# Kernel tuning notes

Hardware: AMD Instinct MI355X
Metric: run time of the kernel (lower is better)

Reference implementation:

```python
import jax, jax.numpy as jnp
import numpy as np

B, S, DIM, NH = 2, 2048, 1536, 12
HD = DIM // NH            # 128
C = HD // 2               # 64 rotary pairs
CF = C - 2 * (C // 3)     # 22 (frame axis)
CH = C // 3               # 21 (height axis)
CW = C // 3               # 21 (width axis)
GF, GH, GW = 8, 16, 16    # grid sizes, GF*GH*GW == S
EPS = 1e-6


def _freq_table(n_pos, dim):
    inv = 1.0 / (10000.0 ** (np.arange(dim, dtype=np.float64) / dim))
    ang = np.outer(np.arange(n_pos, dtype=np.float64), inv)
    return (np.cos(ang).astype(np.float32), np.sin(ang).astype(np.float32))


def setup_inputs() -> dict:
    key = jax.random.key(0)
    ks = jax.random.split(key, 8)
    scale = 0.02
    cos_f, sin_f = _freq_table(GF, CF)
    cos_h, sin_h = _freq_table(GH, CH)
    cos_w, sin_w = _freq_table(GW, CW)
    return {
        'x': jax.random.normal(ks[0], (B, S, DIM), dtype=jnp.float32),
        'seq_lens': jnp.array([2048, 1600], dtype=jnp.int32),
        'f': GF, 'h': GH, 'w': GW,
        'wq': scale * jax.random.normal(ks[1], (DIM, DIM), dtype=jnp.float32),
        'bq': jnp.zeros((DIM,), jnp.float32),
        'wk': scale * jax.random.normal(ks[2], (DIM, DIM), dtype=jnp.float32),
        'bk': jnp.zeros((DIM,), jnp.float32),
        'wv': scale * jax.random.normal(ks[3], (DIM, DIM), dtype=jnp.float32),
        'bv': jnp.zeros((DIM,), jnp.float32),
        'wo': scale * jax.random.normal(ks[4], (DIM, DIM), dtype=jnp.float32),
        'bo': jnp.zeros((DIM,), jnp.float32),
        'nq_w': jnp.ones((DIM,), jnp.float32),
        'nk_w': jnp.ones((DIM,), jnp.float32),
        'cos_f': jnp.asarray(cos_f), 'sin_f': jnp.asarray(sin_f),
        'cos_h': jnp.asarray(cos_h), 'sin_h': jnp.asarray(sin_h),
        'cos_w': jnp.asarray(cos_w), 'sin_w': jnp.asarray(sin_w),
    }


def _rmsnorm(t, wt):
    return t * jax.lax.rsqrt(jnp.mean(t * t, axis=-1, keepdims=True) + EPS) * wt


def _grid_rope(t, cos, sin, b, s):
    # t: [b, s, NH, HD] ; cos/sin: [s, 1, C] (per-position assembled freqs)
    tp = t.reshape(b, s, NH, C, 2)
    xr, xi = tp[..., 0], tp[..., 1]
    rr = xr * cos - xi * sin          # complex multiply by e^{i*theta}
    ri = xr * sin + xi * cos
    return jnp.stack([rr, ri], axis=-1).reshape(b, s, NH, HD)


def reference(x, seq_lens, f, h, w, wq, bq, wk, bk, wv, bv, wo, bo,
              nq_w, nk_w, cos_f, sin_f, cos_h, sin_h, cos_w, sin_w):
    b, s, _ = x.shape
    # QKV projections with RMSNorm on q/k over full dim (as in the module)
    q = _rmsnorm(x @ wq.T + bq, nq_w).reshape(b, s, NH, HD)
    k = _rmsnorm(x @ wk.T + bk, nk_w).reshape(b, s, NH, HD)
    v = (x @ wv.T + bv).reshape(b, s, NH, HD)
    # grid-indexed RoPE: zero offsets / target==grid => arange sampling per axis
    idx = jnp.arange(s)
    fi = idx // (h * w)
    hi = (idx // w) % h
    wi = idx % w
    cos = jnp.concatenate([cos_f[fi], cos_h[hi], cos_w[wi]], axis=-1)[:, None, :]
    sin = jnp.concatenate([sin_f[fi], sin_h[hi], sin_w[wi]], axis=-1)[:, None, :]
    qr = _grid_rope(q, cos, sin, b, s)
    kr = _grid_rope(k, cos, sin, b, s)
    # attention with ragged key-length masking (flash_attention k_lens)
    scale = 1.0 / jnp.sqrt(jnp.float32(HD))
    scores = jnp.einsum('bqnd,bknd->bnqk', qr, kr) * scale
    kmask = idx[None, :] < seq_lens[:, None]            # [b, s]
    scores = jnp.where(kmask[:, None, None, :], scores, jnp.float32(-1e30))
    attn = jax.nn.softmax(scores, axis=-1)
    out = jnp.einsum('bnqk,bknd->bqnd', attn, v).reshape(b, s, DIM)
    return out @ wo.T + bo
```

## Files before the change

kernel.cpp:

```cpp
#include <hip/hip_runtime.h>
#include <hip/hip_bf16.h>
#include <math.h>

#define DIM_  1536
#define NH_   12
#define HD_   128
#define S_    2048
#define B_    2
#define M_    (B_*S_)
#define WEL_  (DIM_*DIM_)

typedef __attribute__((ext_vector_type(8))) _Float16 f16x8;
typedef __attribute__((ext_vector_type(4))) short short4v;
typedef __attribute__((ext_vector_type(8))) short short8v;
typedef __attribute__((ext_vector_type(4))) float f32x4;

#define SSCALE_LOG2E (0.08838834764831845f * 1.4426950408889634f)

static __device__ __forceinline__ short f2h(float f) {
  union { _Float16 h; short s; } u;
  u.h = (_Float16)f;
  return u.s;
}

static __device__ __forceinline__ unsigned pk2h(float a, float b) {
  typedef __attribute__((ext_vector_type(2))) __fp16 fp16x2;
  union { fp16x2 v; unsigned u; } u2;
  u2.v = __builtin_amdgcn_cvt_pkrtz(a, b);
  return u2.u;
}

__global__ __launch_bounds__(256) void f2h_k(
    const float* __restrict__ in, short* __restrict__ out, int n8)
{
  int i = blockIdx.x * 256 + threadIdx.x;
  if (i >= n8) return;
  const float4* p = (const float4*)in + (size_t)i * 2;
  float4 a = p[0], b = p[1];
  short8v o;
  o[0] = f2h(a.x); o[1] = f2h(a.y); o[2] = f2h(a.z); o[3] = f2h(a.w);
  o[4] = f2h(b.x); o[5] = f2h(b.y); o[6] = f2h(b.z); o[7] = f2h(b.w);
  *((short8v*)out + i) = o;
}

__global__ __launch_bounds__(256) void f2h4_k(
    const float* __restrict__ x, const float* __restrict__ wq,
    const float* __restrict__ wk, const float* __restrict__ wv,
    short* __restrict__ x16, short* __restrict__ w16)
{
  int i = blockIdx.x * 256 + threadIdx.x;
  const float* src; short* dst; int j;
  if (i < 786432)       { src = x;  dst = x16;            j = i; }
  else if (i < 1081344) { src = wq; dst = w16;            j = i - 786432; }
  else if (i < 1376256) { src = wk; dst = w16 + WEL_;     j = i - 1081344; }
  else                  { src = wv; dst = w16 + 2 * WEL_; j = i - 1376256; }
  const float4* p = (const float4*)src + (size_t)j * 2;
  float4 a = p[0], b = p[1];
  short8v o;
  o[0] = f2h(a.x); o[1] = f2h(a.y); o[2] = f2h(a.z); o[3] = f2h(a.w);
  o[4] = f2h(b.x); o[5] = f2h(b.y); o[6] = f2h(b.z); o[7] = f2h(b.w);
  *((short8v*)dst + j) = o;
}

template<bool F16OUT>
static __device__ __forceinline__ void gemm16_core(
    const short* __restrict__ A16, const short* __restrict__ W16,
    const float* __restrict__ bias, void* __restrict__ Outp,
    int m0, int n0)
{
  __shared__ __align__(16) char Atile[8192];
  __shared__ __align__(16) char Btile[8192];
  const int tid = threadIdx.x;
  const int l  = tid & 63, w = tid >> 6;
  const int wr = w >> 1, wc = w & 1;
  const int lc = l & 15, lg = l >> 4;

  f32x4 acc[4][4] = {};

  const int rs  = w * 16 + (l >> 2);
  const int gsl = ((l & 3) ^ ((rs >> 1) & 3)) * 8;
  const short* gA0 = A16 + (size_t)(m0 + rs) * DIM_ + gsl;
  const short* gA1 = A16 + (size_t)(m0 + 64 + rs) * DIM_ + gsl;
  const short* gB0 = W16 + (size_t)(n0 + rs) * DIM_ + gsl;
  const short* gB1 = W16 + (size_t)(n0 + 64 + rs) * DIM_ + gsl;

  for (int k0 = 0; k0 < DIM_; k0 += 32) {
    __builtin_amdgcn_global_load_lds(
        (const __attribute__((address_space(1))) unsigned*)(gA0 + k0),
        (__attribute__((address_space(3))) unsigned*)(Atile + w * 1024), 16, 0, 0);
    __builtin_amdgcn_global_load_lds(
        (const __attribute__((address_space(1))) unsigned*)(gA1 + k0),
        (__attribute__((address_space(3))) unsigned*)(Atile + 4096 + w * 1024), 16, 0, 0);
    __builtin_amdgcn_global_load_lds(
        (const __attribute__((address_space(1))) unsigned*)(gB0 + k0),
        (__attribute__((address_space(3))) unsigned*)(Btile + w * 1024), 16, 0, 0);
    __builtin_amdgcn_global_load_lds(
        (const __attribute__((address_space(1))) unsigned*)(gB1 + k0),
        (__attribute__((address_space(3))) unsigned*)(Btile + 4096 + w * 1024), 16, 0, 0);
    __syncthreads();

    f16x8 af[4], bf[4];
#pragma unroll
    for (int mt = 0; mt < 4; ++mt) {
      int ar = wr * 64 + mt * 16 + lc;
      af[mt] = *(const f16x8*)(Atile + ar * 64 + ((lg ^ ((ar >> 1) & 3)) << 4));
    }
#pragma unroll
    for (int nt = 0; nt < 4; ++nt) {
      int br = wc * 64 + nt * 16 + lc;
      bf[nt] = *(const f16x8*)(Btile + br * 64 + ((lg ^ ((br >> 1) & 3)) << 4));
    }
#pragma unroll
    for (int mt = 0; mt < 4; ++mt)
#pragma unroll
      for (int nt = 0; nt < 4; ++nt)
        acc[mt][nt] = __builtin_amdgcn_mfma_f32_16x16x32_f16(af[mt], bf[nt], acc[mt][nt], 0, 0, 0);
    __syncthreads();
  }

#pragma unroll
  for (int nt = 0; nt < 4; ++nt) {
    int col = n0 + wc * 64 + nt * 16 + lc;
    float bb = bias[col];
#pragma unroll
    for (int mt = 0; mt < 4; ++mt) {
#pragma unroll
      for (int r = 0; r < 4; ++r) {
        int rowm = m0 + wr * 64 + mt * 16 + lg * 4 + r;
        if (F16OUT)
          ((short*)Outp)[(size_t)rowm * DIM_ + col] = f2h(acc[mt][nt][r] + bb);
        else
          ((float*)Outp)[(size_t)rowm * DIM_ + col] = acc[mt][nt][r] + bb;
      }
    }
  }
}

__global__ __launch_bounds__(256) void gemm_qk_k(
    const short* __restrict__ x16, const short* __restrict__ w16,
    const float* __restrict__ bq, const float* __restrict__ bk,
    float* __restrict__ qf, float* __restrict__ kf)
{
  const int z = blockIdx.z;
  gemm16_core<false>(x16, w16 + (size_t)z * WEL_, z ? bk : bq,
                     z ? (void*)kf : (void*)qf,
                     blockIdx.y * 128, blockIdx.x * 128);
}

__global__ __launch_bounds__(256) void gemm_v16_k(
    const short* __restrict__ x16, const short* __restrict__ wv16,
    const float* __restrict__ bv, short* __restrict__ vf16)
{
  gemm16_core<true>(x16, wv16, bv, vf16, blockIdx.y * 128, blockIdx.x * 128);
}

__global__ __launch_bounds__(256) void gemm_out16_k(
    const short* __restrict__ att16, const short* __restrict__ wo16,
    const float* __restrict__ bo, float* __restrict__ out)
{
  gemm16_core<false>(att16, wo16, bo, out, blockIdx.y * 128, blockIdx.x * 128);
}

__global__ __launch_bounds__(256) void rms_rope_pack_k(
    const float* __restrict__ t, const float* __restrict__ w,
    const float* __restrict__ cf, const float* __restrict__ sf,
    const float* __restrict__ ch, const float* __restrict__ sh,
    const float* __restrict__ cw, const float* __restrict__ sw,
    short* __restrict__ outb, float qsc)
{
  const int row = blockIdx.x;
  const int b   = row >> 11;
  const int s   = row & (S_ - 1);
  const float* rp = t + (size_t)row * DIM_;

  float ss = 0.f;
  for (int i = threadIdx.x; i < DIM_; i += 256) { float v2 = rp[i]; ss += v2 * v2; }
#pragma unroll
  for (int off = 32; off > 0; off >>= 1) ss += __shfl_down(ss, off);
  __shared__ float red[4];
  if ((threadIdx.x & 63) == 0) red[threadIdx.x >> 6] = ss;
  __syncthreads();
  float scale = rsqrtf((red[0] + red[1] + red[2] + red[3]) * (1.f / DIM_) + 1e-6f) * qsc;

  const int fi = s >> 8;
  const int hi = (s >> 4) & 15;
  const int wi = s & 15;

  for (int p = threadIdx.x; p < NH_ * 64; p += 256) {
    int n = p >> 6, c = p & 63;
    float co, si;
    if (c < 22)      { co = cf[fi * 22 + c];        si = sf[fi * 22 + c]; }
    else if (c < 43) { co = ch[hi * 21 + (c - 22)]; si = sh[hi * 21 + (c - 22)]; }
    else             { co = cw[wi * 21 + (c - 43)]; si = sw[wi * 21 + (c - 43)]; }
    int d0 = n * HD_ + 2 * c;
    float xr = rp[d0]     * scale * w[d0];
    float xi = rp[d0 + 1] * scale * w[d0 + 1];
    float rr = xr * co - xi * si;
    float ri = xr * si + xi * co;
    *(unsigned int*)(outb + (((size_t)(b * NH_ + n) * S_ + s) * HD_ + 2 * c)) = pk2h(rr, ri);
  }
}

__global__ __launch_bounds__(256) void v_transpose16_k(
    const short* __restrict__ v16, short* __restrict__ vtb)
{
  const int bh = blockIdx.y;
  const int b  = bh / NH_;
  const int h  = bh - b * NH_;
  const int s0 = blockIdx.x << 6;
  __shared__ short tile[64][136];
  const int tid = threadIdx.x;
#pragma unroll
  for (int i = 0; i < 4; ++i) {
    int f  = tid + (i << 8);
    int sl = f >> 4, d8 = f & 15;
    short8v v8 = *(const short8v*)(v16 + (size_t)(b * S_ + s0 + sl) * DIM_ + h * 128 + d8 * 8);
#pragma unroll
    for (int j = 0; j < 8; ++j) tile[sl][d8 * 8 + j] = v8[j];
  }
  __syncthreads();
#pragma unroll
  for (int i = 0; i < 4; ++i) {
    int f  = tid + (i << 8);
    int d  = f >> 3, s8 = f & 7;
    short8v o8;
#pragma unroll
    for (int j = 0; j < 8; ++j) o8[j] = tile[s8 * 8 + j][d];
    *(short8v*)(vtb + ((size_t)bh * HD_ + d) * S_ + s0 + s8 * 8) = o8;
  }
}

__global__ __launch_bounds__(256) void attn_mfma5_k(
    const short* __restrict__ qb, const short* __restrict__ kb,
    const short* __restrict__ vtb, const int* __restrict__ seq_lens,
    short* __restrict__ o16)
{
  const int bh = blockIdx.y;
  const int b  = bh / NH_;
  const int h  = bh - b * NH_;
  const int q0 = blockIdx.x << 6;
  const int kvlen = seq_lens[b];
  const int tid  = threadIdx.x;
  const int wid  = tid >> 6;
  const int lane = tid & 63;
  const int lg   = lane >> 4;
  const int lc   = lane & 15;
  const int xo   = (lc & 7) << 4;

  __shared__ __align__(16) char Kt[16384];
  __shared__ __align__(16) char Vt[16384];
  __shared__ __align__(16) char Pt[4][2048];

  f16x8 bq[4];
  {
    const size_t base = ((size_t)bh * S_ + q0 + wid * 16 + lc) * HD_;
#pragma unroll
    for (int dc = 0; dc < 4; ++dc)
      bq[dc] = *(const f16x8*)(qb + base + dc * 32 + lg * 8);
  }

  const short* kgA = kb + ((size_t)bh * S_ + wid * 16 + lg) * HD_
                        + ((lc * 8) ^ (lg << 3));
  const short* kgB = kb + ((size_t)bh * S_ + wid * 16 + 4 + lg) * HD_
                        + ((lc * 8) ^ ((lg ^ 4) << 3));
  const short* vg  = vtb + ((size_t)bh * HD_ + wid * 32 + (lane >> 3)) * S_
                         + (((lane & 7) * 8) ^ ((lane >> 3) << 3));

#define STAGE_K()                                                              \
  {                                                                            \
    _Pragma("unroll")                                                          \
    for (int j = 0; j < 4; ++j) {                                              \
      const short* g = (j & 1) ? (kgB + ((j - 1) >> 1) * (8 * HD_))            \
                               : (kgA + (j >> 1) * (8 * HD_));                 \
      __builtin_amdgcn_global_load_lds(                                        \
          (const __attribute__((address_space(1))) unsigned*)g,                \
          (__attribute__((address_space(3))) unsigned*)(Kt + (wid * 16 + j * 4) * 256), \
          16, 0, 0);                                                           \
    }                                                                          \
  }
#define STAGE_V()                                                              \
  {                                                                            \
    _Pragma("unroll")                                                          \
    for (int j = 0; j < 4; ++j) {                                              \
      __builtin_amdgcn_global_load_lds(                                        \
          (const __attribute__((address_space(1))) unsigned*)(vg + j * 8 * S_),\
          (__attribute__((address_space(3))) unsigned*)(Vt + (wid * 32 + j * 8) * 128), \
          16, 0, 0);                                                           \
    }                                                                          \
  }

  f32x4 oacc[8] = {};
  float m = -3.0e38f, l = 0.f;

  const int nt = kvlen >> 6;

  STAGE_K();
  kgA += 64 * HD_; kgB += 64 * HD_;
  __syncthreads();

  for (int ti = 0; ti < nt; ++ti) {
    STAGE_V();
    vg += 64;

    f32x4 s[4];
    __builtin_amdgcn_s_setprio(1);
#pragma unroll
    for (int kt = 0; kt < 4; ++kt) {
      f32x4 a = {0.f, 0.f, 0.f, 0.f};
      const char* kr = Kt + (kt * 16 + lc) * 256;
#pragma unroll
      for (int dc = 0; dc < 4; ++dc) {
        f16x8 kf = *(const f16x8*)(kr + ((dc * 64 + lg * 16) ^ xo));
        a = __builtin_amdgcn_mfma_f32_16x16x32_f16(kf, bq[dc], a, 0, 0, 0);
      }
      s[kt] = a;
    }
    __builtin_amdgcn_s_setprio(0);

    float t0 = -3.0e38f;
#pragma unroll
    for (int kt = 0; kt < 4; ++kt)
#pragma unroll
      for (int r = 0; r < 4; ++r) t0 = fmaxf(t0, s[kt][r]);
    t0 = fmaxf(t0, __shfl_xor(t0, 16));
    t0 = fmaxf(t0, __shfl_xor(t0, 32));

    if (__any(t0 > m + 8.f)) {
      float mn = fmaxf(m, t0);
      float a  = exp2f(m - mn);
      m = mn; l *= a;
#pragma unroll
      for (int r = 0; r < 4; ++r) {
        float ar = __shfl(a, 4 * lg + r);
#pragma unroll
        for (int n = 0; n < 8; ++n) oacc[n][r] *= ar;
      }
    }
    float ls = 0.f;
#pragma unroll
    for (int kt = 0; kt < 4; ++kt)
#pragma unroll
      for (int r = 0; r < 4; ++r) {
        float p = exp2f(s[kt][r] - m); s[kt][r] = p; ls += p;
      }
    ls += __shfl_xor(ls, 16);
    ls += __shfl_xor(ls, 32);
    l += ls;

    {
      char* pr = Pt[wid] + lc * 128;
#pragma unroll
      for (int kt = 0; kt < 4; ++kt) {
#pragma unroll
        for (int rr = 0; rr < 2; ++rr) {
          unsigned u = pk2h(s[kt][2 * rr], s[kt][2 * rr + 1]);
          int off = (kt * 32 + lg * 8 + rr * 4) ^ xo;
          *(unsigned*)(pr + off) = u;
        }
      }
    }

    __syncthreads();

    if (ti + 1 < nt) {
      STAGE_K();
      kgA += 64 * HD_; kgB += 64 * HD_;
    }

    __builtin_amdgcn_s_setprio(1);
#pragma unroll
    for (int kc = 0; kc < 2; ++kc) {
      f16x8 pa = *(const f16x8*)(Pt[wid] + lc * 128 + ((kc * 64 + lg * 16) ^ xo));
#pragma unroll
      for (int n = 0; n < 8; ++n) {
        f16x8 vf = *(const f16x8*)(Vt + (n * 16 + lc) * 128 + ((kc * 64 + lg * 16) ^ xo));
        oacc[n] = __builtin_amdgcn_mfma_f32_16x16x32_f16(pa, vf, oacc[n], 0, 0, 0);
      }
    }
    __builtin_amdgcn_s_setprio(0);

    __syncthreads();
  }

#pragma unroll
  for (int r = 0; r < 4; ++r) {
    float li = 1.f / __shfl(l, 4 * lg + r);
    int qrow = q0 + wid * 16 + 4 * lg + r;
#pragma unroll
    for (int n = 0; n < 8; ++n)
      o16[((size_t)(b * S_ + qrow) * NH_ + h) * HD_ + n * 16 + lc] = f2h(oacc[n][r] * li);
  }
#undef STAGE_K
#undef STAGE_V
}

extern "C" void kernel_launch(void* const* d_in, const int* in_sizes, int n_in,
                              void* d_out, int out_size, void* d_ws, size_t ws_size,
                              hipStream_t stream) {
  const float* x        = (const float*)d_in[0];
  const int*   seq_lens = (const int*)d_in[1];
  const float* wq = (const float*)d_in[5];
  const float* bq = (const float*)d_in[6];
  const float* wk = (const float*)d_in[7];
  const float* bk = (const float*)d_in[8];
  const float* wv = (const float*)d_in[9];
  const float* bv = (const float*)d_in[10];
  const float* wo = (const float*)d_in[11];
  const float* bo = (const float*)d_in[12];
  const float* nq = (const float*)d_in[13];
  const float* nk = (const float*)d_in[14];
  const float* cf = (const float*)d_in[15];
  const float* sf = (const float*)d_in[16];
  const float* ch = (const float*)d_in[17];
  const float* sh = (const float*)d_in[18];
  const float* cw = (const float*)d_in[19];
  const float* sw = (const float*)d_in[20];

  const size_t rowelems = (size_t)M_ * DIM_;
  float* qf   = (float*)d_ws;
  float* kf   = qf + rowelems;
  short* vf16 = (short*)(kf + rowelems);
  short* x16  = vf16 + rowelems;
  short* w16  = x16 + rowelems;
  short* vt   = x16;
  short* qh   = vf16;
  short* kh   = (short*)d_ws + rowelems;
  short* att16 = (short*)d_ws;
  short* wo16 = (short*)kf;
  float* out  = (float*)d_out;

  f2h4_k<<<6528, 256, 0, stream>>>(x, wq, wk, wv, x16, w16);

  gemm_qk_k<<<dim3(DIM_ / 128, M_ / 128, 2), 256, 0, stream>>>(
      x16, w16, bq, bk, qf, kf);
  gemm_v16_k<<<dim3(DIM_ / 128, M_ / 128), 256, 0, stream>>>(
      x16, w16 + 2 * (size_t)WEL_, bv, vf16);

  v_transpose16_k<<<dim3(S_ / 64, B_ * NH_), 256, 0, stream>>>(vf16, vt);

  rms_rope_pack_k<<<M_, 256, 0, stream>>>(qf, nq, cf, sf, ch, sh, cw, sw, qh,
                                          SSCALE_LOG2E);
  rms_rope_pack_k<<<M_, 256, 0, stream>>>(kf, nk, cf, sf, ch, sh, cw, sw, kh, 1.0f);

  f2h_k<<<1152, 256, 0, stream>>>(wo, wo16, WEL_ / 8);

  attn_mfma5_k<<<dim3(S_ / 64, B_ * NH_), 256, 0, stream>>>(qh, kh, vt, seq_lens, att16);

  gemm_out16_k<<<dim3(DIM_ / 128, M_ / 128), 256, 0, stream>>>(att16, wo16, bo, out);
}
```

Measured before the change: 254.0 us.

## Fuse QKV GEMMs, write V transposed in epilogue, fp16 Q/K intermediates, narrower out GEMM tiles

Merges the Q/K and V projection GEMMs into one launch over three z-slices. The V slice writes its output directly in the transposed per-head layout, which removes the separate transpose kernel. Q and K are now stored as fp16 instead of fp32, halving the traffic into the RMSNorm/RoPE kernels at some cost in precision before normalization. The output GEMM switches to 128x64 tiles to launch more blocks, and the workspace layout is reorganized to fit.

```diff
diff --git a/kernel.cpp b/kernel.cpp
--- a/kernel.cpp
+++ b/kernel.cpp
@@ -62,10 +62,10 @@
   *((short8v*)dst + j) = o;
 }
 
-template<bool F16OUT>
+template<int MODE>
 static __device__ __forceinline__ void gemm16_core(
     const short* __restrict__ A16, const short* __restrict__ W16,
-    const float* __restrict__ bias, void* __restrict__ Outp,
+    const float* __restrict__ bias, short* __restrict__ Outp,
     int m0, int n0)
 {
   __shared__ __align__(16) char Atile[8192];
@@ -118,51 +118,123 @@
     __syncthreads();
   }
 
-#pragma unroll
-  for (int nt = 0; nt < 4; ++nt) {
-    int col = n0 + wc * 64 + nt * 16 + lc;
-    float bb = bias[col];
-#pragma unroll
-    for (int mt = 0; mt < 4; ++mt) {
-#pragma unroll
-      for (int r = 0; r < 4; ++r) {
-        int rowm = m0 + wr * 64 + mt * 16 + lg * 4 + r;
-        if (F16OUT)
-          ((short*)Outp)[(size_t)rowm * DIM_ + col] = f2h(acc[mt][nt][r] + bb);
-        else
-          ((float*)Outp)[(size_t)rowm * DIM_ + col] = acc[mt][nt][r] + bb;
-      }
-    }
-  }
-}
-
-__global__ __launch_bounds__(256) void gemm_qk_k(
+  if (MODE == 0) {
+#pragma unroll
+    for (int nt = 0; nt < 4; ++nt) {
+      int col = n0 + wc * 64 + nt * 16 + lc;
+      float bb = bias[col];
+#pragma unroll
+      for (int mt = 0; mt < 4; ++mt) {
+#pragma unroll
+        for (int r = 0; r < 4; ++r) {
+          int rowm = m0 + wr * 64 + mt * 16 + lg * 4 + r;
+          Outp[(size_t)rowm * DIM_ + col] = f2h(acc[mt][nt][r] + bb);
+        }
+      }
+    }
+  } else {
+#pragma unroll
+    for (int nt = 0; nt < 4; ++nt) {
+      int colg = n0 + wc * 64 + nt * 16 + lc;
+      int h = colg >> 7, d = colg & 127;
+      float bb = bias[colg];
+#pragma unroll
+      for (int mt = 0; mt < 4; ++mt) {
+        int rowg = m0 + wr * 64 + mt * 16 + lg * 4;
+        int b = rowg >> 11, s = rowg & (S_ - 1);
+        short4v o4;
+#pragma unroll
+        for (int r = 0; r < 4; ++r) o4[r] = f2h(acc[mt][nt][r] + bb);
+        *(short4v*)(Outp + ((size_t)((b * NH_ + h) * HD_ + d)) * S_ + s) = o4;
+      }
+    }
+  }
+}
+
+__global__ __launch_bounds__(256) void gemm_qkv16_k(
     const short* __restrict__ x16, const short* __restrict__ w16,
     const float* __restrict__ bq, const float* __restrict__ bk,
-    float* __restrict__ qf, float* __restrict__ kf)
+    const float* __restrict__ bv,
+    short* __restrict__ q16, short* __restrict__ k16, short* __restrict__ vt)
 {
   const int z = blockIdx.z;
-  gemm16_core<false>(x16, w16 + (size_t)z * WEL_, z ? bk : bq,
-                     z ? (void*)kf : (void*)qf,
-                     blockIdx.y * 128, blockIdx.x * 128);
-}
-
-__global__ __launch_bounds__(256) void gemm_v16_k(
-    const short* __restrict__ x16, const short* __restrict__ wv16,
-    const float* __restrict__ bv, short* __restrict__ vf16)
-{
-  gemm16_core<true>(x16, wv16, bv, vf16, blockIdx.y * 128, blockIdx.x * 128);
-}
-
-__global__ __launch_bounds__(256) void gemm_out16_k(
+  if (z == 2)
+    gemm16_core<2>(x16, w16 + 2 * (size_t)WEL_, bv, vt,
+                   blockIdx.y * 128, blockIdx.x * 128);
+  else
+    gemm16_core<0>(x16, w16 + (size_t)z * WEL_, z ? bk : bq, z ? k16 : q16,
+                   blockIdx.y * 128, blockIdx.x * 128);
+}
+
+__global__ __launch_bounds__(256) void gemm_out64_k(
     const short* __restrict__ att16, const short* __restrict__ wo16,
     const float* __restrict__ bo, float* __restrict__ out)
 {
-  gemm16_core<false>(att16, wo16, bo, out, blockIdx.y * 128, blockIdx.x * 128);
-}
-
-__global__ __launch_bounds__(256) void rms_rope_pack_k(
-    const float* __restrict__ t, const float* __restrict__ w,
+  __shared__ __align__(16) char Atile[8192];
+  __shared__ __align__(16) char Btile[4096];
+  const int m0 = blockIdx.y * 128, n0 = blockIdx.x * 64;
+  const int tid = threadIdx.x;
+  const int l  = tid & 63, w = tid >> 6;
+  const int lc = l & 15, lg = l >> 4;
+
+  f32x4 acc[2][4] = {};
+
+  const int rsA = w * 32 + (l >> 2);
+  const int rsB = w * 16 + (l >> 2);
+  const int gslA = ((l & 3) ^ ((rsA >> 1) & 3)) * 8;
+  const int gslB = ((l & 3) ^ ((rsB >> 1) & 3)) * 8;
+  const short* gA0 = att16 + (size_t)(m0 + rsA) * DIM_ + gslA;
+  const short* gA1 = att16 + (size_t)(m0 + 16 + rsA) * DIM_ + gslA;
+  const short* gB0 = wo16 + (size_t)(n0 + rsB) * DIM_ + gslB;
+
+  for (int k0 = 0; k0 < DIM_; k0 += 32) {
+    __builtin_amdgcn_global_load_lds(
+        (const __attribute__((address_space(1))) unsigned*)(gA0 + k0),
+        (__attribute__((address_space(3))) unsigned*)(Atile + w * 2048), 16, 0, 0);
+    __builtin_amdgcn_global_load_lds(
+        (const __attribute__((address_space(1))) unsigned*)(gA1 + k0),
+        (__attribute__((address_space(3))) unsigned*)(Atile + w * 2048 + 1024), 16, 0, 0);
+    __builtin_amdgcn_global_load_lds(
+        (const __attribute__((address_space(1))) unsigned*)(gB0 + k0),
+        (__attribute__((address_space(3))) unsigned*)(Btile + w * 1024), 16, 0, 0);
+    __syncthreads();
+
+    f16x8 af[2], bf[4];
+#pragma unroll
+    for (int mt = 0; mt < 2; ++mt) {
+      int ar = w * 32 + mt * 16 + lc;
+      af[mt] = *(const f16x8*)(Atile + ar * 64 + ((lg ^ ((ar >> 1) & 3)) << 4));
+    }
+#pragma unroll
+    for (int nt = 0; nt < 4; ++nt) {
+      int br = nt * 16 + lc;
+      bf[nt] = *(const f16x8*)(Btile + br * 64 + ((lg ^ ((br >> 1) & 3)) << 4));
+    }
+#pragma unroll
+    for (int mt = 0; mt < 2; ++mt)
+#pragma unroll
+      for (int nt = 0; nt < 4; ++nt)
+        acc[mt][nt] = __builtin_amdgcn_mfma_f32_16x16x32_f16(af[mt], bf[nt], acc[mt][nt], 0, 0, 0);
+    __syncthreads();
+  }
+
+#pragma unroll
+  for (int nt = 0; nt < 4; ++nt) {
+    int col = n0 + nt * 16 + lc;
+    float bb = bo[col];
+#pragma unroll
+    for (int mt = 0; mt < 2; ++mt) {
+#pragma unroll
+      for (int r = 0; r < 4; ++r) {
+        int rowm = m0 + w * 32 + mt * 16 + lg * 4 + r;
+        out[(size_t)rowm * DIM_ + col] = acc[mt][nt][r] + bb;
+      }
+    }
+  }
+}
+
+__global__ __launch_bounds__(256) void rms_rope_pack16_k(
+    const short* __restrict__ t, const float* __restrict__ w,
     const float* __restrict__ cf, const float* __restrict__ sf,
     const float* __restrict__ ch, const float* __restrict__ sh,
     const float* __restrict__ cw, const float* __restrict__ sw,
@@ -171,10 +243,12 @@
   const int row = blockIdx.x;
   const int b   = row >> 11;
   const int s   = row & (S_ - 1);
-  const float* rp = t + (size_t)row * DIM_;
+  const _Float16* rp = (const _Float16*)(t + (size_t)row * DIM_);
 
   float ss = 0.f;
-  for (int i = threadIdx.x; i < DIM_; i += 256) { float v2 = rp[i]; ss += v2 * v2; }
+  for (int i = threadIdx.x; i < DIM_; i += 256) {
+    float v2 = (float)rp[i]; ss += v2 * v2;
+  }
 #pragma unroll
   for (int off = 32; off > 0; off >>= 1) ss += __shfl_down(ss, off);
   __shared__ float red[4];
@@ -193,40 +267,11 @@
     else if (c < 43) { co = ch[hi * 21 + (c - 22)]; si = sh[hi * 21 + (c - 22)]; }
     else             { co = cw[wi * 21 + (c - 43)]; si = sw[wi * 21 + (c - 43)]; }
     int d0 = n * HD_ + 2 * c;
-    float xr = rp[d0]     * scale * w[d0];
-    float xi = rp[d0 + 1] * scale * w[d0 + 1];
+    float xr = (float)rp[d0]     * scale * w[d0];
+    float xi = (float)rp[d0 + 1] * scale * w[d0 + 1];
     float rr = xr * co - xi * si;
     float ri = xr * si + xi * co;
     *(unsigned int*)(outb + (((size_t)(b * NH_ + n) * S_ + s) * HD_ + 2 * c)) = pk2h(rr, ri);
-  }
-}
-
-__global__ __launch_bounds__(256) void v_transpose16_k(
-    const short* __restrict__ v16, short* __restrict__ vtb)
-{
-  const int bh = blockIdx.y;
-  const int b  = bh / NH_;
-  const int h  = bh - b * NH_;
-  const int s0 = blockIdx.x << 6;
-  __shared__ short tile[64][136];
-  const int tid = threadIdx.x;
-#pragma unroll
-  for (int i = 0; i < 4; ++i) {
-    int f  = tid + (i << 8);
-    int sl = f >> 4, d8 = f & 15;
-    short8v v8 = *(const short8v*)(v16 + (size_t)(b * S_ + s0 + sl) * DIM_ + h * 128 + d8 * 8);
-#pragma unroll
-    for (int j = 0; j < 8; ++j) tile[sl][d8 * 8 + j] = v8[j];
-  }
-  __syncthreads();
-#pragma unroll
-  for (int i = 0; i < 4; ++i) {
-    int f  = tid + (i << 8);
-    int d  = f >> 3, s8 = f & 7;
-    short8v o8;
-#pragma unroll
-    for (int j = 0; j < 8; ++j) o8[j] = tile[s8 * 8 + j][d];
-    *(short8v*)(vtb + ((size_t)bh * HD_ + d) * S_ + s0 + s8 * 8) = o8;
   }
 }
 
@@ -417,34 +462,29 @@
   const float* sw = (const float*)d_in[20];
 
   const size_t rowelems = (size_t)M_ * DIM_;
-  float* qf   = (float*)d_ws;
-  float* kf   = qf + rowelems;
-  short* vf16 = (short*)(kf + rowelems);
-  short* x16  = vf16 + rowelems;
-  short* w16  = x16 + rowelems;
-  short* vt   = x16;
-  short* qh   = vf16;
-  short* kh   = (short*)d_ws + rowelems;
-  short* att16 = (short*)d_ws;
-  short* wo16 = (short*)kf;
-  float* out  = (float*)d_out;
+  short* x16 = (short*)d_ws;
+  short* w16 = x16 + rowelems;
+  short* q16 = w16 + 3 * (size_t)WEL_;
+  short* k16 = q16 + rowelems;
+  short* vt  = k16 + rowelems;
+  short* qh  = vt + rowelems;
+  short* kh  = qh + rowelems;
+  short* att16 = q16;
+  short* wo16  = k16;
+  float* out = (float*)d_out;
 
   f2h4_k<<<6528, 256, 0, stream>>>(x, wq, wk, wv, x16, w16);
 
-  gemm_qk_k<<<dim3(DIM_ / 128, M_ / 128, 2), 256, 0, stream>>>(
-      x16, w16, bq, bk, qf, kf);
-  gemm_v16_k<<<dim3(DIM_ / 128, M_ / 128), 256, 0, stream>>>(
-      x16, w16 + 2 * (size_t)WEL_, bv, vf16);
-
-  v_transpose16_k<<<dim3(S_ / 64, B_ * NH_), 256, 0, stream>>>(vf16, vt);
-
-  rms_rope_pack_k<<<M_, 256, 0, stream>>>(qf, nq, cf, sf, ch, sh, cw, sw, qh,
-                                          SSCALE_LOG2E);
-  rms_rope_pack_k<<<M_, 256, 0, stream>>>(kf, nk, cf, sf, ch, sh, cw, sw, kh, 1.0f);
+  gemm_qkv16_k<<<dim3(DIM_ / 128, M_ / 128, 3), 256, 0, stream>>>(
+      x16, w16, bq, bk, bv, q16, k16, vt);
+
+  rms_rope_pack16_k<<<M_, 256, 0, stream>>>(q16, nq, cf, sf, ch, sh, cw, sw, qh,
+                                            SSCALE_LOG2E);
+  rms_rope_pack16_k<<<M_, 256, 0, stream>>>(k16, nk, cf, sf, ch, sh, cw, sw, kh, 1.0f);
 
   f2h_k<<<1152, 256, 0, stream>>>(wo, wo16, WEL_ / 8);
 
   attn_mfma5_k<<<dim3(S_ / 64, B_ * NH_), 256, 0, stream>>>(qh, kh, vt, seq_lens, att16);
 
-  gemm_out16_k<<<dim3(DIM_ / 128, M_ / 128), 256, 0, stream>>>(att16, wo16, bo, out);
-}
+  gemm_out64_k<<<dim3(DIM_ / 64, M_ / 128), 256, 0, stream>>>(att16, wo16, bo, out);
+}
```

Result: no change. 257.0 us (+1.2%).
